# Kernel tuning notes

Hardware: AMD Instinct MI355X
Metric: run time of the kernel (lower is better)

## Reference

```python
import jax, jax.numpy as jnp
import numpy as np

NUM_NODES = 10000  # fixed by input spec: edge_index values in [0, 10000)


def setup_inputs() -> dict:
    key = jax.random.key(0)
    k1, k2, k3 = jax.random.split(key, 3)
    N, E, D_IN, D_OUT = NUM_NODES, 320000, 256, 256
    x = jax.random.normal(k1, (N, D_IN), dtype=jnp.float32)
    edge_index = jax.random.randint(k2, (2, E), 0, N, dtype=jnp.int64)
    # ensure node N-1 appears so num_nodes == N as in the torch code
    edge_index = edge_index.at[0, 0].set(N - 1)
    # xavier_uniform for [D_IN, D_OUT]
    limit = float(np.sqrt(6.0 / (D_IN + D_OUT)))
    weight = jax.random.uniform(k3, (D_IN, D_OUT), dtype=jnp.float32,
                                minval=-limit, maxval=limit)
    return {"x": x, "edge_index": edge_index, "weight": weight}


def _normalize_adjacency(edge_index, num_nodes):
    src, dst = edge_index[0], edge_index[1]
    ones = jnp.ones(src.shape[0], dtype=jnp.float32)
    # symmetric binarized adjacency: adj[i,j] = adj[j,i] = 1 (set, not add)
    adj = jnp.zeros((num_nodes, num_nodes), dtype=jnp.float32)
    adj = adj.at[src, dst].max(ones)
    adj = adj.at[dst, src].max(ones)
    # one round of self-loops: adj += I
    adj = adj + jnp.eye(num_nodes, dtype=jnp.float32)
    deg = jnp.sum(adj, axis=1)                    # [N]
    dinv = 1.0 / jnp.sqrt(deg)                    # [N]
    # D^-1/2 A D^-1/2 via broadcasting (equivalent to diag mms)
    return adj * dinv[:, None] * dinv[None, :]


def reference(x, edge_index, weight):
    adj = _normalize_adjacency(edge_index, NUM_NODES)  # [N, N]
    h = adj @ x                                        # [N, D_IN]
    return h @ weight                                  # [N, D_OUT]
```

## Files before the change

kernel.cpp:

```cpp
#include <hip/hip_runtime.h>
#include <hip/hip_bf16.h>
#include <stdint.h>

#define N_NODES   10000
#define D_FEAT    256
#define E_EDGES   320000
#define ROW_WORDS 313
#define ROW_STRIDE 320
#define LIST_CAP  1024

#define NB     1000
#define RPB    10
#define B_CAP  1024
#define NBLK_E 313
#define NBLK_W 64
#define NBLK_C 1000
#define NBLK_G 625
#define COLSTR 128

#define LDSTR 264

typedef __attribute__((ext_vector_type(4))) float float4v;
typedef _Float16 half8  __attribute__((ext_vector_type(8)));
typedef _Float16 half4v __attribute__((ext_vector_type(4)));

__device__ __forceinline__ float h2f_lo(uint32_t u) {
    union { uint32_t u; _Float16 h[2]; } v; v.u = u; return (float)v.h[0];
}
__device__ __forceinline__ float h2f_hi(uint32_t u) {
    union { uint32_t u; _Float16 h[2]; } v; v.u = u; return (float)v.h[1];
}


__global__ void __launch_bounds__(1024)
fill_sort(const int* __restrict__ ei, uint32_t* __restrict__ bucketbuf,
          uint32_t* __restrict__ cursors,
          const float* __restrict__ w, _Float16* __restrict__ wt) {
    __shared__ uint32_t hist[1024];
    __shared__ uint32_t lofs[1024];
    __shared__ uint32_t base_s[1024];
    __shared__ uint32_t stage[2048];
    __shared__ uint16_t sbkt[2048];
    int t = threadIdx.x;

    if (blockIdx.x >= NBLK_E) {
        int kb = (blockIdx.x - NBLK_E) * 4;
        int k = kb + (t >> 8), n = t & 255;
        float* st = (float*)stage;
        st[(n << 2) | (t >> 8)] = w[(size_t)k * D_FEAT + n];
        __syncthreads();
        if (t < 256) {
            half4v o = { (_Float16)st[t * 4 + 0], (_Float16)st[t * 4 + 1],
                         (_Float16)st[t * 4 + 2], (_Float16)st[t * 4 + 3] };
            *(half4v*)&wt[(size_t)t * D_FEAT + kb] = o;
        }
        return;
    }

    hist[t] = 0;
    __syncthreads();
    int e = blockIdx.x * 1024 + t;
    int b0 = -1, b1 = -1; uint32_t ent0 = 0, ent1 = 0, s0 = 0, s1 = 0;
    if (e < E_EDGES) {
        int s = ei[e], d = ei[E_EDGES + e];
        if ((uint32_t)s < N_NODES && (uint32_t)d < N_NODES) {
            b0 = s / RPB; ent0 = ((uint32_t)(s - b0 * RPB) << 14) | (uint32_t)d;
            b1 = d / RPB; ent1 = ((uint32_t)(d - b1 * RPB) << 14) | (uint32_t)s;
            s0 = atomicAdd(&hist[b0], 1u);
            s1 = atomicAdd(&hist[b1], 1u);
        }
    }
    __syncthreads();
    lofs[t] = hist[t];
    __syncthreads();
    for (int d = 1; d < 1024; d <<= 1) {
        uint32_t v = (t >= d) ? lofs[t - d] : 0;
        __syncthreads();
        lofs[t] += v;
        __syncthreads();
    }
    base_s[t] = hist[t] ? atomicAdd(&cursors[t], hist[t]) : 0u;
    if (b0 >= 0) {
        uint32_t p0 = lofs[b0] - hist[b0] + s0;
        stage[p0] = ent0; sbkt[p0] = (uint16_t)b0;
        uint32_t p1 = lofs[b1] - hist[b1] + s1;
        stage[p1] = ent1; sbkt[p1] = (uint16_t)b1;
    }
    __syncthreads();
    uint32_t total = lofs[1023];
    for (uint32_t idx = t; idx < total; idx += 1024) {
        uint32_t b = sbkt[idx];
        uint32_t pos = base_s[b] + (idx - (lofs[b] - hist[b]));
        if (pos < B_CAP) bucketbuf[(size_t)b * B_CAP + pos] = stage[idx];
    }
}

__global__ void __launch_bounds__(1024)
csr_gemm(const uint32_t* __restrict__ bucketbuf, const uint32_t* __restrict__ cursors,
         uint32_t* __restrict__ row_deg, float* __restrict__ dinv,
         uint16_t* __restrict__ col,
         const float* __restrict__ x, const _Float16* __restrict__ wt,
         _Float16* __restrict__ yw) {
    __shared__ __align__(16) uint32_t smem[RPB * ROW_WORDS];
    int t = threadIdx.x;

    if (blockIdx.x >= NBLK_C) {
        _Float16* a_lds = (_Float16*)smem;
        int r0 = (blockIdx.x - NBLK_C) * 16;
        int row = t >> 6, c4 = (t & 63) * 4;
        float4v xv = *(const float4v*)(x + (size_t)(r0 + row) * D_FEAT + c4);
        half4v h = { (_Float16)xv[0], (_Float16)xv[1],
                     (_Float16)xv[2], (_Float16)xv[3] };
        *(half4v*)&a_lds[row * LDSTR + c4] = h;
        __syncthreads();
        int wv = t >> 6, lane = t & 63;
        int quad = lane >> 4, r = lane & 15;
        int ct = wv;
        const _Float16* pb = wt + (size_t)(ct * 16 + r) * D_FEAT + quad * 8;
        float4v acc = {0.f, 0.f, 0.f, 0.f};
        #pragma unroll
        for (int kk = 0; kk < D_FEAT; kk += 32) {
            half8 a = *(const half8*)&a_lds[r * LDSTR + kk + quad * 8];
            half8 b = *(const half8*)(pb + kk);
            acc = __builtin_amdgcn_mfma_f32_16x16x32_f16(a, b, acc, 0, 0, 0);
        }
        int colg = ct * 16 + r;
        #pragma unroll
        for (int u = 0; u < 4; u++)
            yw[(size_t)(r0 + quad * 4 + u) * D_FEAT + colg] = (_Float16)acc[u];
        return;
    }

    uint32_t* bm = smem;
    int b = blockIdx.x;
    for (int i = t; i < RPB * ROW_WORDS; i += 1024) bm[i] = 0;
    __syncthreads();
    uint32_t cnt = min(cursors[b], (uint32_t)B_CAP);
    const uint32_t* bb = bucketbuf + (size_t)b * B_CAP;
    for (uint32_t i = t; i < cnt; i += 1024) {
        uint32_t ent = bb[i];
        uint32_t lr = ent >> 14, d = ent & 0x3FFFu;
        atomicOr(&bm[lr * ROW_WORDS + (d >> 5)], 1u << (d & 31));
    }
    __syncthreads();
    int wv = t >> 6, lane = t & 63;
    if (wv < RPB) {
        int r = wv;
        int gi = b * RPB + r;
        uint32_t wb[5]; int tot = 0;
        #pragma unroll
        for (int k = 0; k < 5; k++) {
            int w = lane + 64 * k;
            uint32_t v = (w < ROW_WORDS) ? bm[r * ROW_WORDS + w] : 0u;
            wb[k] = v; tot += __popc(v);
        }
        int incl = tot;
        #pragma unroll
        for (int off = 1; off < 64; off <<= 1) {
            int v = __shfl_up(incl, off, 64);
            if (lane >= off) incl += v;
        }
        uint32_t total = (uint32_t)__shfl(incl, 63, 64);
        if (lane == 0) {
            row_deg[gi] = min(total, (uint32_t)COLSTR);
            dinv[gi]    = 1.0f / sqrtf((float)(total + 1u));
        }
        uint32_t p = (uint32_t)(incl - tot);
        #pragma unroll
        for (int k = 0; k < 5; k++) {
            uint32_t bits = wb[k];
            uint32_t cbase = (uint32_t)(lane + 64 * k) << 5;
            while (bits) {
                if (p < COLSTR)
                    col[(size_t)gi * COLSTR + p] =
                        (uint16_t)(cbase + (uint32_t)__builtin_ctz(bits));
                p++;
                bits &= bits - 1;
            }
        }
    }
}

__global__ void __launch_bounds__(256)
spmm_out(const uint32_t* __restrict__ row_deg, const float* __restrict__ dinv,
         const uint16_t* __restrict__ col, const _Float16* __restrict__ ywp,
         float* __restrict__ out) {
    const uint16_t* yw = (const uint16_t*)ywp;
    int wv = threadIdx.x >> 6, lane = threadIdx.x & 63;
    int i = blockIdx.x * 4 + wv;
    uint32_t base = (uint32_t)i * COLSTR;
    uint32_t deg = min(row_deg[i], (uint32_t)COLSTR);
    float di = dinv[i];
    float4v z = {0.f, 0.f, 0.f, 0.f};
    float4v a0 = z, a1 = z, a2 = z, a3 = z, a4 = z, a5 = z, a6 = z, a7 = z;
    size_t ch = (size_t)lane * 4;
    uint32_t t8 = deg & ~7u;
    uint32_t t = 0;
    for (; t < t8; t += 8) {
        uint4 cv = *(const uint4*)&col[base + t];
        uint32_t j0 = cv.x & 0xffffu, j1 = cv.x >> 16;
        uint32_t j2 = cv.y & 0xffffu, j3 = cv.y >> 16;
        uint32_t j4 = cv.z & 0xffffu, j5 = cv.z >> 16;
        uint32_t j6 = cv.w & 0xffffu, j7 = cv.w >> 16;
        float d0 = dinv[j0], d1 = dinv[j1], d2 = dinv[j2], d3 = dinv[j3];
        float d4 = dinv[j4], d5 = dinv[j5], d6 = dinv[j6], d7 = dinv[j7];
        uint2 g0 = *(const uint2*)(yw + (size_t)j0 * D_FEAT + ch);
        uint2 g1 = *(const uint2*)(yw + (size_t)j1 * D_FEAT + ch);
        uint2 g2 = *(const uint2*)(yw + (size_t)j2 * D_FEAT + ch);
        uint2 g3 = *(const uint2*)(yw + (size_t)j3 * D_FEAT + ch);
        uint2 g4 = *(const uint2*)(yw + (size_t)j4 * D_FEAT + ch);
        uint2 g5 = *(const uint2*)(yw + (size_t)j5 * D_FEAT + ch);
        uint2 g6 = *(const uint2*)(yw + (size_t)j6 * D_FEAT + ch);
        uint2 g7 = *(const uint2*)(yw + (size_t)j7 * D_FEAT + ch);
        a0[0] += d0 * h2f_lo(g0.x); a0[1] += d0 * h2f_hi(g0.x);
        a0[2] += d0 * h2f_lo(g0.y); a0[3] += d0 * h2f_hi(g0.y);
        a1[0] += d1 * h2f_lo(g1.x); a1[1] += d1 * h2f_hi(g1.x);
        a1[2] += d1 * h2f_lo(g1.y); a1[3] += d1 * h2f_hi(g1.y);
        a2[0] += d2 * h2f_lo(g2.x); a2[1] += d2 * h2f_hi(g2.x);
        a2[2] += d2 * h2f_lo(g2.y); a2[3] += d2 * h2f_hi(g2.y);
        a3[0] += d3 * h2f_lo(g3.x); a3[1] += d3 * h2f_hi(g3.x);
        a3[2] += d3 * h2f_lo(g3.y); a3[3] += d3 * h2f_hi(g3.y);
        a4[0] += d4 * h2f_lo(g4.x); a4[1] += d4 * h2f_hi(g4.x);
        a4[2] += d4 * h2f_lo(g4.y); a4[3] += d4 * h2f_hi(g4.y);
        a5[0] += d5 * h2f_lo(g5.x); a5[1] += d5 * h2f_hi(g5.x);
        a5[2] += d5 * h2f_lo(g5.y); a5[3] += d5 * h2f_hi(g5.y);
        a6[0] += d6 * h2f_lo(g6.x); a6[1] += d6 * h2f_hi(g6.x);
        a6[2] += d6 * h2f_lo(g6.y); a6[3] += d6 * h2f_hi(g6.y);
        a7[0] += d7 * h2f_lo(g7.x); a7[1] += d7 * h2f_hi(g7.x);
        a7[2] += d7 * h2f_lo(g7.y); a7[3] += d7 * h2f_hi(g7.y);
    }
    for (; t < deg; t++) {
        uint32_t j = col[base + t];
        float dj = dinv[j];
        uint2 g = *(const uint2*)(yw + (size_t)j * D_FEAT + ch);
        a0[0] += dj * h2f_lo(g.x); a0[1] += dj * h2f_hi(g.x);
        a0[2] += dj * h2f_lo(g.y); a0[3] += dj * h2f_hi(g.y);
    }
    uint2 gs = *(const uint2*)(yw + (size_t)i * D_FEAT + ch);
    a1[0] += di * h2f_lo(gs.x); a1[1] += di * h2f_hi(gs.x);
    a1[2] += di * h2f_lo(gs.y); a1[3] += di * h2f_hi(gs.y);
    float4v acc = ((a0 + a1) + (a2 + a3)) + ((a4 + a5) + (a6 + a7));
    *(float4v*)(out + (size_t)i * D_FEAT + ch) = di * acc;
}


__global__ void scatter_edges_fb(const int* __restrict__ ei,
                                 uint32_t* __restrict__ bitmap) {
    int e = blockIdx.x * blockDim.x + threadIdx.x;
    if (e >= E_EDGES) return;
    int s = ei[e], d = ei[E_EDGES + e];
    if ((uint32_t)s >= N_NODES || (uint32_t)d >= N_NODES) return;
    atomicOr(&bitmap[(size_t)s * ROW_STRIDE + (d >> 5)], 1u << (d & 31));
    atomicOr(&bitmap[(size_t)d * ROW_STRIDE + (s >> 5)], 1u << (s & 31));
}

__global__ void __launch_bounds__(256)
popc_dinv(const uint32_t* __restrict__ bitmap, float* __restrict__ dinv) {
    int wv = threadIdx.x >> 6, lane = threadIdx.x & 63;
    int i = blockIdx.x * 4 + wv;
    const uint32_t* rb = bitmap + (size_t)i * ROW_STRIDE;
    int pop = 0;
    #pragma unroll
    for (int k = 0; k < 5; k++) {
        int w = lane + 64 * k;
        if (w < ROW_WORDS) pop += __popc(rb[w]);
    }
    #pragma unroll
    for (int off = 32; off > 0; off >>= 1) pop += __shfl_xor(pop, off, 64);
    if (lane == 0) dinv[i] = 1.0f / sqrtf((float)(pop + 1));
}

__global__ void __launch_bounds__(256)
spmm_bitmap_fb(const uint32_t* __restrict__ bitmap, const float* __restrict__ dinv,
               const float* __restrict__ xf, float* __restrict__ agg) {
    __shared__ __align__(16) uint32_t lists[4][LIST_CAP];
    int wv = threadIdx.x >> 6, lane = threadIdx.x & 63;
    int i = blockIdx.x * 4 + wv;
    uint32_t* list = lists[wv];
    const uint32_t* rb = bitmap + (size_t)i * ROW_STRIDE;

    uint32_t wbits[5]; int tot = 0;
    #pragma unroll
    for (int k = 0; k < 5; k++) {
        int w = lane + 64 * k;
        uint32_t b = (w < ROW_WORDS) ? rb[w] : 0u;
        wbits[k] = b;
        tot += __popc(b);
    }
    int incl = tot;
    #pragma unroll
    for (int off = 1; off < 64; off <<= 1) {
        int v = __shfl_up(incl, off, 64);
        if (lane >= off) incl += v;
    }
    uint32_t p = (uint32_t)(incl - tot);
    uint32_t deg = (uint32_t)__shfl(incl, 63, 64);
    #pragma unroll
    for (int k = 0; k < 5; k++) {
        uint32_t bits = wbits[k];
        uint32_t base = (uint32_t)(lane + 64 * k) << 5;
        while (bits) {
            if (p < LIST_CAP) list[p] = base + (uint32_t)__builtin_ctz(bits);
            p++;
            bits &= bits - 1;
        }
    }
    if (deg > LIST_CAP) deg = LIST_CAP;

    float di = dinv[i];
    float4v z = {0.f, 0.f, 0.f, 0.f};
    float4v acc0 = z, acc1 = z, acc2 = z, acc3 = z;
    float4v sv = *(const float4v*)(xf + (size_t)i * D_FEAT + lane * 4);
    uint32_t t4 = deg & ~3u;
    for (uint32_t k = 0; k < t4; k += 4) {
        uint4 jv = *(const uint4*)&list[k];
        float d0 = dinv[jv.x], d1 = dinv[jv.y], d2 = dinv[jv.z], d3 = dinv[jv.w];
        float4v v0 = *(const float4v*)(xf + (size_t)jv.x * D_FEAT + lane * 4);
        float4v v1 = *(const float4v*)(xf + (size_t)jv.y * D_FEAT + lane * 4);
        float4v v2 = *(const float4v*)(xf + (size_t)jv.z * D_FEAT + lane * 4);
        float4v v3 = *(const float4v*)(xf + (size_t)jv.w * D_FEAT + lane * 4);
        acc0 += d0 * v0; acc1 += d1 * v1; acc2 += d2 * v2; acc3 += d3 * v3;
    }
    for (uint32_t k = t4; k < deg; k++) {
        uint32_t j = list[k];
        acc0 += dinv[j] * (*(const float4v*)(xf + (size_t)j * D_FEAT + lane * 4));
    }
    float4v acc = (acc0 + acc1) + (acc2 + acc3) + di * sv;
    *(float4v*)(agg + (size_t)i * D_FEAT + lane * 4) = di * acc;
}

__global__ void __launch_bounds__(256)
gemm_valu(float* __restrict__ io, const float* __restrict__ wf) {
    __shared__ __align__(16) float a_lds[16 * D_FEAT];
    int c = threadIdx.x;
    int r0 = blockIdx.x * 16;
    for (int idx = c; idx < 16 * D_FEAT; idx += 256)
        a_lds[idx] = io[(size_t)r0 * D_FEAT + idx];
    __syncthreads();
    float acc[16];
    #pragma unroll
    for (int r = 0; r < 16; r++) acc[r] = 0.f;
    for (int k0 = 0; k0 < D_FEAT; k0 += 4) {
        float w0 = wf[(size_t)(k0 + 0) * D_FEAT + c];
        float w1 = wf[(size_t)(k0 + 1) * D_FEAT + c];
        float w2 = wf[(size_t)(k0 + 2) * D_FEAT + c];
        float w3 = wf[(size_t)(k0 + 3) * D_FEAT + c];
        #pragma unroll
        for (int r = 0; r < 16; r++) {
            float4v av = *(const float4v*)&a_lds[r * D_FEAT + k0];
            acc[r] = fmaf(av[3], w3, fmaf(av[2], w2,
                     fmaf(av[1], w1, fmaf(av[0], w0, acc[r]))));
        }
    }
    #pragma unroll
    for (int r = 0; r < 16; r++)
        io[(size_t)(r0 + r) * D_FEAT + c] = acc[r];
}

extern "C" void kernel_launch(void* const* d_in, const int* in_sizes, int n_in,
                              void* d_out, int out_size, void* d_ws, size_t ws_size,
                              hipStream_t stream) {
    const float* x  = (const float*)d_in[0];
    const int*   ei = (const int*)d_in[1];
    const float* w  = (const float*)d_in[2];
    float* out = (float*)d_out;
    uint8_t* ws = (uint8_t*)d_ws;

    const size_t BB_OFF   = 4096;
    const size_t RD_OFF   = 4100096;
    const size_t DI_OFF   = 4140096;
    const size_t WT_OFF   = 4180096;
    const size_t YW_OFF   = 4311168;
    const size_t COL_OFF  = 9431168;
    const size_t NEED_NEW = 11991168;
    const size_t NEED_FB  = 12840000;

    if (ws_size >= NEED_NEW) {
        uint32_t* cursors   = (uint32_t*)ws;
        uint32_t* bucketbuf = (uint32_t*)(ws + BB_OFF);
        uint32_t* row_deg   = (uint32_t*)(ws + RD_OFF);
        float*    dinv      = (float*)(ws + DI_OFF);
        _Float16* wt        = (_Float16*)(ws + WT_OFF);
        _Float16* yw        = (_Float16*)(ws + YW_OFF);
        uint16_t* col       = (uint16_t*)(ws + COL_OFF);

        hipMemsetAsync(cursors, 0, 4096, stream);
        fill_sort<<<NBLK_E + NBLK_W, 1024, 0, stream>>>(ei, bucketbuf, cursors, w, wt);
        csr_gemm <<<NBLK_C + NBLK_G, 1024, 0, stream>>>(bucketbuf, cursors,
                                                        row_deg, dinv, col, x, wt, yw);
        spmm_out <<<N_NODES / 4, 256, 0, stream>>>(row_deg, dinv, col, yw, out);
    } else if (ws_size >= NEED_FB) {
        uint32_t* bitmap = (uint32_t*)ws;
        float*    dinv   = (float*)(ws + 12800000);

        hipMemsetAsync(bitmap, 0, 12800000, stream);
        scatter_edges_fb<<<(E_EDGES + 255) / 256, 256, 0, stream>>>(ei, bitmap);
        popc_dinv      <<<N_NODES / 4, 256, 0, stream>>>(bitmap, dinv);
        spmm_bitmap_fb <<<N_NODES / 4, 256, 0, stream>>>(bitmap, dinv, x, out);
        gemm_valu      <<<N_NODES / 16, 256, 0, stream>>>(out, w);
    }
}
```

Baseline: 132.4 us.

## Widen SpMM gathers to 16-byte loads with half-wave edge split; shuffle-based bucket scan

The SpMM kernel now splits each wave into two halves that handle alternating groups of 8 neighbours. Each lane gathers 8 fp16 features with one 16-byte load, and the next column indices are prefetched. A cross-half shuffle reduction combines the partial sums. Separately, the bucketing kernel replaces its barrier-heavy Hillis-Steele LDS scan with a wave-shuffle scan plus a small cross-wave pass. The cost is more registers (16 float4 accumulators) and some padded gathers masked to zero weight when the degree is not a multiple of 16.

```diff
diff --git a/kernel.cpp b/kernel.cpp
--- a/kernel.cpp
+++ b/kernel.cpp
@@ -39,6 +39,7 @@
     __shared__ uint32_t hist[1024];
     __shared__ uint32_t lofs[1024];
     __shared__ uint32_t base_s[1024];
+    __shared__ uint32_t wsum[16];
     __shared__ uint32_t stage[2048];
     __shared__ uint16_t sbkt[2048];
     int t = threadIdx.x;
@@ -57,6 +58,7 @@
         return;
     }
 
+    int wv = t >> 6, lane = t & 63;
     hist[t] = 0;
     __syncthreads();
     int e = blockIdx.x * 1024 + t;
@@ -71,15 +73,29 @@
         }
     }
     __syncthreads();
-    lofs[t] = hist[t];
-    __syncthreads();
-    for (int d = 1; d < 1024; d <<= 1) {
-        uint32_t v = (t >= d) ? lofs[t - d] : 0;
-        __syncthreads();
-        lofs[t] += v;
-        __syncthreads();
-    }
-    base_s[t] = hist[t] ? atomicAdd(&cursors[t], hist[t]) : 0u;
+    uint32_t h = hist[t];
+    uint32_t incl = h;
+    #pragma unroll
+    for (int off = 1; off < 64; off <<= 1) {
+        uint32_t v = __shfl_up(incl, off, 64);
+        if (lane >= off) incl += v;
+    }
+    if (lane == 63) wsum[wv] = incl;
+    __syncthreads();
+    if (wv == 0) {
+        uint32_t s = (lane < 16) ? wsum[lane] : 0u;
+        #pragma unroll
+        for (int off = 1; off < 16; off <<= 1) {
+            uint32_t v = __shfl_up(s, off, 64);
+            if (lane >= off) s += v;
+        }
+        if (lane < 16) wsum[lane] = s;
+    }
+    __syncthreads();
+    uint32_t wbase = wv ? wsum[wv - 1] : 0u;
+    lofs[t] = incl + wbase;
+    base_s[t] = h ? atomicAdd(&cursors[t], h) : 0u;
+    __syncthreads();
     if (b0 >= 0) {
         uint32_t p0 = lofs[b0] - hist[b0] + s0;
         stage[p0] = ent0; sbkt[p0] = (uint16_t)b0;
@@ -187,60 +203,70 @@
          float* __restrict__ out) {
     const uint16_t* yw = (const uint16_t*)ywp;
     int wv = threadIdx.x >> 6, lane = threadIdx.x & 63;
+    int half = lane >> 5, sl = lane & 31;
     int i = blockIdx.x * 4 + wv;
     uint32_t base = (uint32_t)i * COLSTR;
     uint32_t deg = min(row_deg[i], (uint32_t)COLSTR);
     float di = dinv[i];
+    size_t ch = (size_t)sl * 8;
     float4v z = {0.f, 0.f, 0.f, 0.f};
-    float4v a0 = z, a1 = z, a2 = z, a3 = z, a4 = z, a5 = z, a6 = z, a7 = z;
-    size_t ch = (size_t)lane * 4;
-    uint32_t t8 = deg & ~7u;
-    uint32_t t = 0;
-    for (; t < t8; t += 8) {
-        uint4 cv = *(const uint4*)&col[base + t];
-        uint32_t j0 = cv.x & 0xffffu, j1 = cv.x >> 16;
-        uint32_t j2 = cv.y & 0xffffu, j3 = cv.y >> 16;
-        uint32_t j4 = cv.z & 0xffffu, j5 = cv.z >> 16;
-        uint32_t j6 = cv.w & 0xffffu, j7 = cv.w >> 16;
-        float d0 = dinv[j0], d1 = dinv[j1], d2 = dinv[j2], d3 = dinv[j3];
-        float d4 = dinv[j4], d5 = dinv[j5], d6 = dinv[j6], d7 = dinv[j7];
-        uint2 g0 = *(const uint2*)(yw + (size_t)j0 * D_FEAT + ch);
-        uint2 g1 = *(const uint2*)(yw + (size_t)j1 * D_FEAT + ch);
-        uint2 g2 = *(const uint2*)(yw + (size_t)j2 * D_FEAT + ch);
-        uint2 g3 = *(const uint2*)(yw + (size_t)j3 * D_FEAT + ch);
-        uint2 g4 = *(const uint2*)(yw + (size_t)j4 * D_FEAT + ch);
-        uint2 g5 = *(const uint2*)(yw + (size_t)j5 * D_FEAT + ch);
-        uint2 g6 = *(const uint2*)(yw + (size_t)j6 * D_FEAT + ch);
-        uint2 g7 = *(const uint2*)(yw + (size_t)j7 * D_FEAT + ch);
-        a0[0] += d0 * h2f_lo(g0.x); a0[1] += d0 * h2f_hi(g0.x);
-        a0[2] += d0 * h2f_lo(g0.y); a0[3] += d0 * h2f_hi(g0.y);
-        a1[0] += d1 * h2f_lo(g1.x); a1[1] += d1 * h2f_hi(g1.x);
-        a1[2] += d1 * h2f_lo(g1.y); a1[3] += d1 * h2f_hi(g1.y);
-        a2[0] += d2 * h2f_lo(g2.x); a2[1] += d2 * h2f_hi(g2.x);
-        a2[2] += d2 * h2f_lo(g2.y); a2[3] += d2 * h2f_hi(g2.y);
-        a3[0] += d3 * h2f_lo(g3.x); a3[1] += d3 * h2f_hi(g3.x);
-        a3[2] += d3 * h2f_lo(g3.y); a3[3] += d3 * h2f_hi(g3.y);
-        a4[0] += d4 * h2f_lo(g4.x); a4[1] += d4 * h2f_hi(g4.x);
-        a4[2] += d4 * h2f_lo(g4.y); a4[3] += d4 * h2f_hi(g4.y);
-        a5[0] += d5 * h2f_lo(g5.x); a5[1] += d5 * h2f_hi(g5.x);
-        a5[2] += d5 * h2f_lo(g5.y); a5[3] += d5 * h2f_hi(g5.y);
-        a6[0] += d6 * h2f_lo(g6.x); a6[1] += d6 * h2f_hi(g6.x);
-        a6[2] += d6 * h2f_lo(g6.y); a6[3] += d6 * h2f_hi(g6.y);
-        a7[0] += d7 * h2f_lo(g7.x); a7[1] += d7 * h2f_hi(g7.x);
-        a7[2] += d7 * h2f_lo(g7.y); a7[3] += d7 * h2f_hi(g7.y);
-    }
-    for (; t < deg; t++) {
-        uint32_t j = col[base + t];
-        float dj = dinv[j];
-        uint2 g = *(const uint2*)(yw + (size_t)j * D_FEAT + ch);
-        a0[0] += dj * h2f_lo(g.x); a0[1] += dj * h2f_hi(g.x);
-        a0[2] += dj * h2f_lo(g.y); a0[3] += dj * h2f_hi(g.y);
-    }
-    uint2 gs = *(const uint2*)(yw + (size_t)i * D_FEAT + ch);
-    a1[0] += di * h2f_lo(gs.x); a1[1] += di * h2f_hi(gs.x);
-    a1[2] += di * h2f_lo(gs.y); a1[3] += di * h2f_hi(gs.y);
-    float4v acc = ((a0 + a1) + (a2 + a3)) + ((a4 + a5) + (a6 + a7));
-    *(float4v*)(out + (size_t)i * D_FEAT + ch) = di * acc;
+    float4v accl[8], acch[8];
+    #pragma unroll
+    for (int k = 0; k < 8; k++) { accl[k] = z; acch[k] = z; }
+
+    uint32_t hb = (uint32_t)(half << 3);
+    uint4 cv = {0u, 0u, 0u, 0u};
+    if (deg) cv = *(const uint4*)&col[base + hb];
+
+    for (uint32_t t = 0; t < deg; t += 16) {
+        uint4 cvn = {0u, 0u, 0u, 0u};
+        uint32_t tn = t + 16;
+        if (tn < deg) cvn = *(const uint4*)&col[base + tn + hb];
+        uint32_t tb = t + hb;
+        uint32_t jr[8];
+        jr[0] = cv.x & 0xffffu; jr[1] = cv.x >> 16;
+        jr[2] = cv.y & 0xffffu; jr[3] = cv.y >> 16;
+        jr[4] = cv.z & 0xffffu; jr[5] = cv.z >> 16;
+        jr[6] = cv.w & 0xffffu; jr[7] = cv.w >> 16;
+        uint4 g[8]; float dk[8];
+        #pragma unroll
+        for (int k = 0; k < 8; k++) {
+            uint32_t j = min(jr[k], (uint32_t)(N_NODES - 1));
+            g[k]  = *(const uint4*)(yw + ((size_t)j << 8) + ch);
+            dk[k] = dinv[j];
+        }
+        #pragma unroll
+        for (int k = 0; k < 8; k++) {
+            float d = (tb + (uint32_t)k < deg) ? dk[k] : 0.f;
+            accl[k][0] += d * h2f_lo(g[k].x); accl[k][1] += d * h2f_hi(g[k].x);
+            accl[k][2] += d * h2f_lo(g[k].y); accl[k][3] += d * h2f_hi(g[k].y);
+            acch[k][0] += d * h2f_lo(g[k].z); acch[k][1] += d * h2f_hi(g[k].z);
+            acch[k][2] += d * h2f_lo(g[k].w); acch[k][3] += d * h2f_hi(g[k].w);
+        }
+        cv = cvn;
+    }
+
+    if (half == 0) {
+        const uint4 gs = *(const uint4*)(yw + ((size_t)i << 8) + ch);
+        accl[0][0] += di * h2f_lo(gs.x); accl[0][1] += di * h2f_hi(gs.x);
+        accl[0][2] += di * h2f_lo(gs.y); accl[0][3] += di * h2f_hi(gs.y);
+        acch[0][0] += di * h2f_lo(gs.z); acch[0][1] += di * h2f_hi(gs.z);
+        acch[0][2] += di * h2f_lo(gs.w); acch[0][3] += di * h2f_hi(gs.w);
+    }
+
+    float4v lo = ((accl[0] + accl[1]) + (accl[2] + accl[3])) +
+                 ((accl[4] + accl[5]) + (accl[6] + accl[7]));
+    float4v hi = ((acch[0] + acch[1]) + (acch[2] + acch[3])) +
+                 ((acch[4] + acch[5]) + (acch[6] + acch[7]));
+    #pragma unroll
+    for (int u = 0; u < 4; u++) {
+        lo[u] += __shfl_xor(lo[u], 32, 64);
+        hi[u] += __shfl_xor(hi[u], 32, 64);
+    }
+    float4v res;
+    if (half) res = hi; else res = lo;
+    float* op = out + (size_t)i * D_FEAT + (size_t)sl * 8 + (half ? 4 : 0);
+    *(float4v*)op = di * res;
 }
 
 
```

After: 132.7 us. Within noise of the previous version (+0.3%).
